# Kernel tuning notes

Measured on AMD Instinct MI355X. Metric: run time of the kernel, lower is better.

The kernel has to match this reference:

```python
import jax, jax.numpy as jnp
import numpy as np

D_MODEL = 1024
DK = 1024
DV = 1024
B, S = 8, 2048


def setup_inputs() -> dict:
    key = jax.random.key(0)
    ks = jax.random.split(key, 7)
    lim = 1.0 / np.sqrt(D_MODEL)
    x = jax.random.normal(ks[0], (B, S, D_MODEL), dtype=jnp.float32)
    Wq = jax.random.uniform(ks[1], (D_MODEL, DK), minval=-lim, maxval=lim, dtype=jnp.float32)
    bq = jax.random.uniform(ks[2], (DK,), minval=-lim, maxval=lim, dtype=jnp.float32)
    Wk = jax.random.uniform(ks[3], (D_MODEL, DK), minval=-lim, maxval=lim, dtype=jnp.float32)
    bk = jax.random.uniform(ks[4], (DK,), minval=-lim, maxval=lim, dtype=jnp.float32)
    Wv = jax.random.uniform(ks[5], (D_MODEL, DV), minval=-lim, maxval=lim, dtype=jnp.float32)
    bv = jax.random.uniform(ks[6], (DV,), minval=-lim, maxval=lim, dtype=jnp.float32)
    return {"x": x, "Wq": Wq, "bq": bq, "Wk": Wk, "bk": bk, "Wv": Wv, "bv": bv}


def reference(x, Wq, bq, Wk, bk, Wv, bv):
    # QKV projections: [B,S,d_model] -> [B,S,dk/dv]
    q = jnp.einsum('bsd,dk->bsk', x, Wq) + bq
    k = jnp.einsum('bsd,dk->bsk', x, Wk) + bk
    v = jnp.einsum('bsd,dv->bsv', x, Wv) + bv
    scale = 1.0 / jnp.sqrt(jnp.float32(DK))
    # scores: [B,S,S]
    scores = jnp.einsum('bqk,bsk->bqs', q, k) * scale
    probs = jax.nn.softmax(scores, axis=-1)
    return jnp.einsum('bqs,bsv->bqv', probs, v)
```

## Files before the change

### kernel.cpp

```cpp
#include <hip/hip_runtime.h>


#define DEV __device__ __forceinline__

typedef unsigned short u16;
typedef __attribute__((ext_vector_type(8))) short bf16x8;
typedef __attribute__((ext_vector_type(4))) float f32x4;

DEV float bf2f(u16 u) {
  unsigned v = ((unsigned)u) << 16;
  float f;
  __builtin_memcpy(&f, &v, 4);
  return f;
}
DEV u16 f2bf(float f) {
  unsigned v;
  __builtin_memcpy(&v, &f, 4);
  return (u16)((v + 0x7fffu + ((v >> 16) & 1u)) >> 16);
}

DEV void gload16(const u16* g, u16* l) {
  __builtin_amdgcn_global_load_lds(
      (const __attribute__((address_space(1))) void*)g,
      (__attribute__((address_space(3))) void*)l, 16, 0, 0);
}

#define BAR() __builtin_amdgcn_s_barrier()
#define SCHED0() __builtin_amdgcn_sched_barrier(0)
#define LGKM0() asm volatile("s_waitcnt lgkmcnt(0)" ::: "memory")
#define VMC(n) asm volatile("s_waitcnt vmcnt(" #n ")" ::: "memory")

__global__ __launch_bounds__(256) void cvt_f32_bf16(const float* __restrict__ x,
                                                    u16* __restrict__ y) {
  const long long i = ((long long)blockIdx.x * 256 + threadIdx.x) * 4;
  float4 v = *(const float4*)&x[i];
  ushort4 o;
  o.x = f2bf(v.x); o.y = f2bf(v.y); o.z = f2bf(v.z); o.w = f2bf(v.w);
  *(ushort4*)&y[i] = o;
}

__global__ __launch_bounds__(256) void transpose_cvt3(
    const float* __restrict__ Wq, const float* __restrict__ Wk,
    const float* __restrict__ Wv, u16* __restrict__ Wt) {
  __shared__ float tl[64][65];
  const float* W = blockIdx.z == 0 ? Wq : blockIdx.z == 1 ? Wk : Wv;
  u16* dst = Wt + (long long)blockIdx.z * 1048576LL;
  const int n0 = blockIdx.x * 64;
  const int k0 = blockIdx.y * 64;
  const int tid = threadIdx.x;
  const int c = tid & 31, r = tid >> 5;
#pragma unroll
  for (int i = 0; i < 8; ++i) {
    const int k = i * 8 + r;
    float2 v2 = *(const float2*)&W[(long long)(k0 + k) * 1024 + n0 + c * 2];
    tl[k][c * 2] = v2.x;
    tl[k][c * 2 + 1] = v2.y;
  }
  __syncthreads();
#pragma unroll
  for (int i = 0; i < 8; ++i) {
    const int n = i * 8 + r;
    ushort2 o;
    o.x = f2bf(tl[c * 2][n]);
    o.y = f2bf(tl[c * 2 + 1][n]);
    *(ushort2*)&dst[(long long)(n0 + n) * 1024 + k0 + c * 2] = o;
  }
}

__global__ __launch_bounds__(256) void reduce_ml(const float* __restrict__ PS,
                                                 float* __restrict__ Li) {
  const int i = blockIdx.x * 256 + threadIdx.x;
  const int z = i >> 11, r = i & 2047;
  const float* ps = PS + ((long long)(z * 8) << 11) + r;
  float L = 0.f;
#pragma unroll
  for (int p = 0; p < 8; ++p) L += ps[p << 11];
  Li[i] = 1.0f / L;
}


template <int OUT_MODE>
__global__ __launch_bounds__(512, 4) void gemm128(
    const u16* __restrict__ A, const u16* __restrict__ B,
    const float* __restrict__ bias, void* __restrict__ Cv, int K, int lda,
    int ldb, int ldc, long long bA, long long bB, long long bC, float scale,
    const float* __restrict__ pm, float* __restrict__ ps) {
  __shared__ __attribute__((aligned(16))) char smem[49152];
  const int tid = threadIdx.x;
  const int w = tid >> 6, l = tid & 63;
  const int wr = w >> 2, wc = w & 3;

  const int gx = gridDim.x, gy = gridDim.y;
  long long flat =
      blockIdx.x + (long long)gx * (blockIdx.y + (long long)gy * blockIdx.z);
  const long long nwg = (long long)gx * gy * gridDim.z;
  if ((nwg & 7) == 0) flat = (flat & 7) * (nwg >> 3) + (flat >> 3);
  const int bx = (int)(flat % gx);
  const long long rem = flat / gx;
  const int by = (int)(rem % gy);
  const int z = (int)(rem / gy);

  A += (long long)z * bA;
  B += (long long)z * bB;
  const long long tm = (long long)by * 128;
  const long long tn = (long long)bx * 256;

  const int l15 = l & 15, hi4 = l >> 4;
  const int slotc = (hi4 ^ ((l15 >> 1) & 3)) * 16;
  const char* bA0 = smem + (wr * 64 + l15) * 64 + slotc;
  const char* bB0 = smem + 8192 + (wc * 64 + l15) * 64 + slotc;

  const int srow = tid >> 2;
  const int kseg = (tid & 3) ^ ((tid >> 3) & 3);
  const int tid16 = tid * 16;
  const u16* pA = A + (tm + srow) * (long long)lda + kseg * 8;
  const u16* pB0 = B + (tn + srow) * (long long)ldb + kseg * 8;
  const u16* pB1 = B + (tn + 128 + srow) * (long long)ldb + kseg * 8;

#define STG(BO)                                           \
  gload16(pA, (u16*)(smem + (BO) + tid16));               \
  gload16(pB0, (u16*)(smem + (BO) + 8192 + tid16));       \
  gload16(pB1, (u16*)(smem + (BO) + 16384 + tid16));      \
  pA += 32;                                               \
  pB0 += 32;                                              \
  pB1 += 32;

#define RDAB(BO)                                                    \
  _Pragma("unroll") for (int mi = 0; mi < 4; ++mi)                  \
      afr[mi] = *(const bf16x8*)(bA0 + (BO) + mi * 1024);           \
  _Pragma("unroll") for (int ni = 0; ni < 4; ++ni)                  \
      bfr[ni] = *(const bf16x8*)(bB0 + (BO) + ni * 1024);

#define MFMAT()                                                          \
  __builtin_amdgcn_s_setprio(1);                                         \
  _Pragma("unroll") for (int ni = 0; ni < 4; ++ni)                       \
      _Pragma("unroll") for (int mi = 0; mi < 4; ++mi)                   \
          acc[mi][ni] = __builtin_amdgcn_mfma_f32_16x16x32_bf16(         \
              afr[mi], bfr[ni], acc[mi][ni], 0, 0, 0);                   \
  __builtin_amdgcn_s_setprio(0);

#define TILE(BO, T)                  \
  RDAB(BO);                          \
  LGKM0();                           \
  SCHED0();                          \
  BAR();                             \
  if ((T) + 2 < nt) {                \
    STG(BO);                         \
    VMC(3);                          \
  } else {                           \
    VMC(0);                          \
  }                                  \
  SCHED0();                          \
  MFMAT();                           \
  SCHED0();                          \
  BAR();

  f32x4 acc[4][4];
  const f32x4 zero = {0.f, 0.f, 0.f, 0.f};
#pragma unroll
  for (int i = 0; i < 4; ++i)
#pragma unroll
    for (int j = 0; j < 4; ++j) acc[i][j] = zero;

  bf16x8 afr[4], bfr[4];
  const int nt = K >> 5;

  STG(0);
  STG(24576);
  VMC(3);
  BAR();

  for (int t = 0; t < nt; t += 2) {
    TILE(0, t);
    TILE(24576, t + 1);
  }

  const int ro4 = (l >> 4) * 4;
  const int co = l & 15;
  if (OUT_MODE == 4) {
    float* C = (float*)Cv + (long long)z * bC;
#pragma unroll
    for (int mi = 0; mi < 4; ++mi) {
      const long long row0 = tm + wr * 64 + mi * 16 + ro4;
      float li[4];
#pragma unroll
      for (int r = 0; r < 4; ++r) li[r] = pm[(long long)z * 2048 + row0 + r];
#pragma unroll
      for (int ni = 0; ni < 4; ++ni) {
        const long long col = tn + wc * 64 + ni * 16 + co;
#pragma unroll
        for (int r = 0; r < 4; ++r)
          C[(row0 + r) * ldc + col] = acc[mi][ni][r] * li[r];
      }
    }
  } else if (OUT_MODE == 1) {
    u16* C = (u16*)Cv + (long long)z * bC;
    float* lps = (float*)smem;
#pragma unroll
    for (int mi = 0; mi < 4; ++mi) {
      const long long row0 = tm + wr * 64 + mi * 16 + ro4;
#pragma unroll
      for (int r = 0; r < 4; ++r) {
        float s_ = 0.f;
#pragma unroll
        for (int ni = 0; ni < 4; ++ni) {
          const float e = __builtin_amdgcn_exp2f(acc[mi][ni][r] * scale);
          s_ += e;
          C[(row0 + r) * ldc + tn + wc * 64 + ni * 16 + co] = f2bf(e);
        }
#pragma unroll
        for (int off = 1; off < 16; off <<= 1) s_ += __shfl_xor(s_, off, 64);
        if (co == 0) lps[(wr * 64 + mi * 16 + ro4 + r) * 4 + wc] = s_;
      }
    }
    __syncthreads();
    if (tid < 128) {
      const float S = lps[tid * 4] + lps[tid * 4 + 1] + lps[tid * 4 + 2] +
                      lps[tid * 4 + 3];
      ps[(((long long)z * 8 + bx) << 11) + tm + tid] = S;
    }
  } else {
    u16* C = (u16*)Cv + (long long)z * bC;
#pragma unroll
    for (int mi = 0; mi < 4; ++mi) {
      const long long row0 = tm + wr * 64 + mi * 16 + ro4;
#pragma unroll
      for (int ni = 0; ni < 4; ++ni) {
        const long long col = tn + wc * 64 + ni * 16 + co;
        const float badd = (OUT_MODE == 0) ? bias[col] : 0.f;
#pragma unroll
        for (int r = 0; r < 4; ++r) {
          float v = acc[mi][ni][r];
          if (OUT_MODE == 0) v += badd;
          if (OUT_MODE == 3) v += bias[row0 + r];
          C[(row0 + r) * ldc + col] = f2bf(v);
        }
      }
    }
  }
}

extern "C" void kernel_launch(void* const* d_in, const int* in_sizes, int n_in,
                              void* d_out, int out_size, void* d_ws,
                              size_t ws_size, hipStream_t stream) {
  const float* x = (const float*)d_in[0];
  const float* Wq = (const float*)d_in[1];
  const float* bq = (const float*)d_in[2];
  const float* Wk = (const float*)d_in[3];
  const float* bk = (const float*)d_in[4];
  const float* Wv = (const float*)d_in[5];
  const float* bv = (const float*)d_in[6];
  float* out = (float*)d_out;

  const long long MT = 16384LL;
  const long long D = 1024LL;

  u16* ws = (u16*)d_ws;
  u16* Wt = ws;
  u16* Q = Wt + 3 * 1048576LL;
  u16* Kb = Q + MT * D;
  u16* Vt = Kb + MT * D;
  u16* SC = Vt + MT * D;
  u16* xb = SC;
  float* PSa = (float*)d_ws;
  float* Li = PSa + 131072;

  const float cl2e = 1.4426950408889634f * 0.03125f;

  cvt_f32_bf16<<<dim3(16384), dim3(256), 0, stream>>>(x, xb);
  transpose_cvt3<<<dim3(16, 16, 3), dim3(256), 0, stream>>>(Wq, Wk, Wv, Wt);
  gemm128<0><<<dim3(4, 128, 1), dim3(512), 0, stream>>>(
      xb, Wt, bq, Q, 1024, 1024, 1024, 1024, 0, 0, 0, 0.f, nullptr, nullptr);
  gemm128<0><<<dim3(4, 128, 1), dim3(512), 0, stream>>>(
      xb, Wt + 1048576LL, bk, Kb, 1024, 1024, 1024, 1024, 0, 0, 0, 0.f,
      nullptr, nullptr);
  gemm128<3><<<dim3(64, 8, 1), dim3(512), 0, stream>>>(
      Wt + 2097152LL, xb, bv, Vt, 1024, 1024, 1024, 16384, 0, 0, 0, 0.f,
      nullptr, nullptr);
  gemm128<1><<<dim3(8, 16, 8), dim3(512), 0, stream>>>(
      Q, Kb, nullptr, SC, 1024, 1024, 1024, 2048, 2048 * 1024LL, 2048 * 1024LL,
      2048LL * 2048LL, cl2e, nullptr, PSa);
  reduce_ml<<<dim3(64), dim3(256), 0, stream>>>(PSa, Li);
  gemm128<4><<<dim3(4, 16, 8), dim3(512), 0, stream>>>(
      SC, Vt, nullptr, out, 2048, 2048, 16384, 1024, 2048LL * 2048LL, 2048LL,
      2048 * 1024LL, 0.f, Li, nullptr);
}
```

Baseline: 299.5 us.

## Switch GEMMs to 32x32x16 MFMA, merge prep kernels and Q/K launches

The GEMM inner loop moves from 16x16x32 bf16 MFMAs to 32x32x16 MFMAs, with 2x2 f32x16 accumulators per wave. LDS fragment reads and all epilogues are remapped to the 32x32 output layout, which needs fewer LDS reads per flop and fewer MFMA issues. The x conversion and the weight transpose-convert are fused into one prep kernel. The Q and K projections run as one batched launch, with the bias pointer picked by z. The 32-lane row layout changes how stores coalesce in the epilogues, and the softmax row sum now needs a wider shuffle reduction.

```diff
diff --git a/kernel.cpp b/kernel.cpp
--- a/kernel.cpp
+++ b/kernel.cpp
@@ -5,7 +5,7 @@
 
 typedef unsigned short u16;
 typedef __attribute__((ext_vector_type(8))) short bf16x8;
-typedef __attribute__((ext_vector_type(4))) float f32x4;
+typedef __attribute__((ext_vector_type(16))) float f32x16;
 
 DEV float bf2f(u16 u) {
   unsigned v = ((unsigned)u) << 16;
@@ -30,24 +30,27 @@
 #define LGKM0() asm volatile("s_waitcnt lgkmcnt(0)" ::: "memory")
 #define VMC(n) asm volatile("s_waitcnt vmcnt(" #n ")" ::: "memory")
 
-__global__ __launch_bounds__(256) void cvt_f32_bf16(const float* __restrict__ x,
-                                                    u16* __restrict__ y) {
-  const long long i = ((long long)blockIdx.x * 256 + threadIdx.x) * 4;
-  float4 v = *(const float4*)&x[i];
-  ushort4 o;
-  o.x = f2bf(v.x); o.y = f2bf(v.y); o.z = f2bf(v.z); o.w = f2bf(v.w);
-  *(ushort4*)&y[i] = o;
-}
-
-__global__ __launch_bounds__(256) void transpose_cvt3(
-    const float* __restrict__ Wq, const float* __restrict__ Wk,
-    const float* __restrict__ Wv, u16* __restrict__ Wt) {
+__global__ __launch_bounds__(256) void prep(const float* __restrict__ x,
+                                            const float* __restrict__ Wq,
+                                            const float* __restrict__ Wk,
+                                            const float* __restrict__ Wv,
+                                            u16* __restrict__ xb,
+                                            u16* __restrict__ Wt) {
   __shared__ float tl[64][65];
-  const float* W = blockIdx.z == 0 ? Wq : blockIdx.z == 1 ? Wk : Wv;
-  u16* dst = Wt + (long long)blockIdx.z * 1048576LL;
-  const int n0 = blockIdx.x * 64;
-  const int k0 = blockIdx.y * 64;
   const int tid = threadIdx.x;
+  if (blockIdx.x < 16384) {
+    const long long i = ((long long)blockIdx.x * 256 + tid) * 4;
+    float4 v = *(const float4*)&x[i];
+    ushort4 o;
+    o.x = f2bf(v.x); o.y = f2bf(v.y); o.z = f2bf(v.z); o.w = f2bf(v.w);
+    *(ushort4*)&xb[i] = o;
+    return;
+  }
+  const int b = blockIdx.x - 16384;
+  const int bz = b >> 8, byk = (b >> 4) & 15, bxn = b & 15;
+  const float* W = bz == 0 ? Wq : bz == 1 ? Wk : Wv;
+  u16* dst = Wt + (long long)bz * 1048576LL;
+  const int n0 = bxn * 64, k0 = byk * 64;
   const int c = tid & 31, r = tid >> 5;
 #pragma unroll
   for (int i = 0; i < 8; ++i) {
@@ -80,7 +83,7 @@
 
 
 template <int OUT_MODE>
-__global__ __launch_bounds__(512, 4) void gemm128(
+__global__ __launch_bounds__(512, 4) void gemm32(
     const u16* __restrict__ A, const u16* __restrict__ B,
     const float* __restrict__ bias, void* __restrict__ Cv, int K, int lda,
     int ldb, int ldc, long long bA, long long bB, long long bC, float scale,
@@ -105,10 +108,12 @@
   const long long tm = (long long)by * 128;
   const long long tn = (long long)bx * 256;
 
-  const int l15 = l & 15, hi4 = l >> 4;
-  const int slotc = (hi4 ^ ((l15 >> 1) & 3)) * 16;
-  const char* bA0 = smem + (wr * 64 + l15) * 64 + slotc;
-  const char* bB0 = smem + 8192 + (wc * 64 + l15) * 64 + slotc;
+  const int l31 = l & 31, h = l >> 5;
+  const int xsw = (l31 >> 1) & 3;
+  const int sl0 = ((0 * 2 + h) ^ xsw) * 16;
+  const int sl1 = ((1 * 2 + h) ^ xsw) * 16;
+  const char* bAr = smem + (wr * 64 + l31) * 64;
+  const char* bBr = smem + 8192 + (wc * 64 + l31) * 64;
 
   const int srow = tid >> 2;
   const int kseg = (tid & 3) ^ ((tid >> 3) & 3);
@@ -125,18 +130,25 @@
   pB0 += 32;                                              \
   pB1 += 32;
 
-#define RDAB(BO)                                                    \
-  _Pragma("unroll") for (int mi = 0; mi < 4; ++mi)                  \
-      afr[mi] = *(const bf16x8*)(bA0 + (BO) + mi * 1024);           \
-  _Pragma("unroll") for (int ni = 0; ni < 4; ++ni)                  \
-      bfr[ni] = *(const bf16x8*)(bB0 + (BO) + ni * 1024);
-
-#define MFMAT()                                                          \
-  __builtin_amdgcn_s_setprio(1);                                         \
-  _Pragma("unroll") for (int ni = 0; ni < 4; ++ni)                       \
-      _Pragma("unroll") for (int mi = 0; mi < 4; ++mi)                   \
-          acc[mi][ni] = __builtin_amdgcn_mfma_f32_16x16x32_bf16(         \
-              afr[mi], bfr[ni], acc[mi][ni], 0, 0, 0);                   \
+#define RDAB(BO)                                            \
+  afr[0][0] = *(const bf16x8*)(bAr + (BO) + sl0);           \
+  afr[0][1] = *(const bf16x8*)(bAr + (BO) + sl1);           \
+  afr[1][0] = *(const bf16x8*)(bAr + (BO) + 2048 + sl0);    \
+  afr[1][1] = *(const bf16x8*)(bAr + (BO) + 2048 + sl1);    \
+  bfr[0][0] = *(const bf16x8*)(bBr + (BO) + sl0);           \
+  bfr[0][1] = *(const bf16x8*)(bBr + (BO) + sl1);           \
+  bfr[1][0] = *(const bf16x8*)(bBr + (BO) + 2048 + sl0);    \
+  bfr[1][1] = *(const bf16x8*)(bBr + (BO) + 2048 + sl1);
+
+#define MFMAT()                                                           \
+  __builtin_amdgcn_s_setprio(1);                                          \
+  _Pragma("unroll") for (int ni = 0; ni < 2; ++ni)                        \
+      _Pragma("unroll") for (int mi = 0; mi < 2; ++mi) {                  \
+    acc[mi][ni] = __builtin_amdgcn_mfma_f32_32x32x16_bf16(                \
+        afr[mi][0], bfr[ni][0], acc[mi][ni], 0, 0, 0);                    \
+    acc[mi][ni] = __builtin_amdgcn_mfma_f32_32x32x16_bf16(                \
+        afr[mi][1], bfr[ni][1], acc[mi][ni], 0, 0, 0);                    \
+  }                                                                       \
   __builtin_amdgcn_s_setprio(0);
 
 #define TILE(BO, T)                  \
@@ -155,14 +167,15 @@
   SCHED0();                          \
   BAR();
 
-  f32x4 acc[4][4];
-  const f32x4 zero = {0.f, 0.f, 0.f, 0.f};
-#pragma unroll
-  for (int i = 0; i < 4; ++i)
-#pragma unroll
-    for (int j = 0; j < 4; ++j) acc[i][j] = zero;
-
-  bf16x8 afr[4], bfr[4];
+  f32x16 acc[2][2];
+#pragma unroll
+  for (int i = 0; i < 2; ++i)
+#pragma unroll
+    for (int j = 0; j < 2; ++j)
+#pragma unroll
+      for (int e = 0; e < 16; ++e) acc[i][j][e] = 0.f;
+
+  bf16x8 afr[2][2], bfr[2][2];
   const int nt = K >> 5;
 
   STG(0);
@@ -175,42 +188,45 @@
     TILE(24576, t + 1);
   }
 
-  const int ro4 = (l >> 4) * 4;
-  const int co = l & 15;
   if (OUT_MODE == 4) {
     float* C = (float*)Cv + (long long)z * bC;
 #pragma unroll
-    for (int mi = 0; mi < 4; ++mi) {
-      const long long row0 = tm + wr * 64 + mi * 16 + ro4;
-      float li[4];
-#pragma unroll
-      for (int r = 0; r < 4; ++r) li[r] = pm[(long long)z * 2048 + row0 + r];
-#pragma unroll
-      for (int ni = 0; ni < 4; ++ni) {
-        const long long col = tn + wc * 64 + ni * 16 + co;
-#pragma unroll
-        for (int r = 0; r < 4; ++r)
-          C[(row0 + r) * ldc + col] = acc[mi][ni][r] * li[r];
+    for (int mi = 0; mi < 2; ++mi) {
+      const long long rb = tm + wr * 64 + mi * 32;
+      float lir[16];
+#pragma unroll
+      for (int rg = 0; rg < 16; ++rg)
+        lir[rg] = pm[(long long)z * 2048 + rb + (rg & 3) + 8 * (rg >> 2) + 4 * h];
+#pragma unroll
+      for (int ni = 0; ni < 2; ++ni) {
+        const long long col = tn + wc * 64 + ni * 32 + l31;
+#pragma unroll
+        for (int rg = 0; rg < 16; ++rg) {
+          const long long row = rb + (rg & 3) + 8 * (rg >> 2) + 4 * h;
+          C[row * ldc + col] = acc[mi][ni][rg] * lir[rg];
+        }
       }
     }
   } else if (OUT_MODE == 1) {
     u16* C = (u16*)Cv + (long long)z * bC;
     float* lps = (float*)smem;
 #pragma unroll
-    for (int mi = 0; mi < 4; ++mi) {
-      const long long row0 = tm + wr * 64 + mi * 16 + ro4;
-#pragma unroll
-      for (int r = 0; r < 4; ++r) {
+    for (int mi = 0; mi < 2; ++mi) {
+      const long long rb = tm + wr * 64 + mi * 32;
+#pragma unroll
+      for (int rg = 0; rg < 16; ++rg) {
+        const int rloc = (rg & 3) + 8 * (rg >> 2) + 4 * h;
+        const long long row = rb + rloc;
         float s_ = 0.f;
 #pragma unroll
-        for (int ni = 0; ni < 4; ++ni) {
-          const float e = __builtin_amdgcn_exp2f(acc[mi][ni][r] * scale);
+        for (int ni = 0; ni < 2; ++ni) {
+          const float e = __builtin_amdgcn_exp2f(acc[mi][ni][rg] * scale);
           s_ += e;
-          C[(row0 + r) * ldc + tn + wc * 64 + ni * 16 + co] = f2bf(e);
+          C[row * ldc + tn + wc * 64 + ni * 32 + l31] = f2bf(e);
         }
 #pragma unroll
-        for (int off = 1; off < 16; off <<= 1) s_ += __shfl_xor(s_, off, 64);
-        if (co == 0) lps[(wr * 64 + mi * 16 + ro4 + r) * 4 + wc] = s_;
+        for (int off = 1; off < 32; off <<= 1) s_ += __shfl_xor(s_, off, 64);
+        if (l31 == 0) lps[(wr * 64 + mi * 32 + rloc) * 4 + wc] = s_;
       }
     }
     __syncthreads();
@@ -219,21 +235,36 @@
                       lps[tid * 4 + 3];
       ps[(((long long)z * 8 + bx) << 11) + tm + tid] = S;
     }
+  } else if (OUT_MODE == 0) {
+    u16* C = (u16*)Cv + (long long)z * bC;
+    const float* bb = z ? pm : bias;
+#pragma unroll
+    for (int mi = 0; mi < 2; ++mi) {
+      const long long rb = tm + wr * 64 + mi * 32;
+#pragma unroll
+      for (int ni = 0; ni < 2; ++ni) {
+        const long long col = tn + wc * 64 + ni * 32 + l31;
+        const float badd = bb[col];
+#pragma unroll
+        for (int rg = 0; rg < 16; ++rg) {
+          const long long row = rb + (rg & 3) + 8 * (rg >> 2) + 4 * h;
+          C[row * ldc + col] = f2bf(acc[mi][ni][rg] + badd);
+        }
+      }
+    }
   } else {
     u16* C = (u16*)Cv + (long long)z * bC;
 #pragma unroll
-    for (int mi = 0; mi < 4; ++mi) {
-      const long long row0 = tm + wr * 64 + mi * 16 + ro4;
-#pragma unroll
-      for (int ni = 0; ni < 4; ++ni) {
-        const long long col = tn + wc * 64 + ni * 16 + co;
-        const float badd = (OUT_MODE == 0) ? bias[col] : 0.f;
-#pragma unroll
-        for (int r = 0; r < 4; ++r) {
-          float v = acc[mi][ni][r];
-          if (OUT_MODE == 0) v += badd;
-          if (OUT_MODE == 3) v += bias[row0 + r];
-          C[(row0 + r) * ldc + col] = f2bf(v);
+    for (int mi = 0; mi < 2; ++mi) {
+      const long long rb = tm + wr * 64 + mi * 32;
+#pragma unroll
+      for (int rg = 0; rg < 16; ++rg) {
+        const long long row = rb + (rg & 3) + 8 * (rg >> 2) + 4 * h;
+        const float badd = bias[row];
+#pragma unroll
+        for (int ni = 0; ni < 2; ++ni) {
+          const long long col = tn + wc * 64 + ni * 32 + l31;
+          C[row * ldc + col] = f2bf(acc[mi][ni][rg] + badd);
         }
       }
     }
@@ -267,21 +298,18 @@
 
   const float cl2e = 1.4426950408889634f * 0.03125f;
 
-  cvt_f32_bf16<<<dim3(16384), dim3(256), 0, stream>>>(x, xb);
-  transpose_cvt3<<<dim3(16, 16, 3), dim3(256), 0, stream>>>(Wq, Wk, Wv, Wt);
-  gemm128<0><<<dim3(4, 128, 1), dim3(512), 0, stream>>>(
-      xb, Wt, bq, Q, 1024, 1024, 1024, 1024, 0, 0, 0, 0.f, nullptr, nullptr);
-  gemm128<0><<<dim3(4, 128, 1), dim3(512), 0, stream>>>(
-      xb, Wt + 1048576LL, bk, Kb, 1024, 1024, 1024, 1024, 0, 0, 0, 0.f,
-      nullptr, nullptr);
-  gemm128<3><<<dim3(64, 8, 1), dim3(512), 0, stream>>>(
+  prep<<<dim3(16384 + 768), dim3(256), 0, stream>>>(x, Wq, Wk, Wv, xb, Wt);
+  gemm32<0><<<dim3(4, 128, 2), dim3(512), 0, stream>>>(
+      xb, Wt, bq, Q, 1024, 1024, 1024, 1024, 0, 1048576LL, 16777216LL, 0.f,
+      bk, nullptr);
+  gemm32<3><<<dim3(64, 8, 1), dim3(512), 0, stream>>>(
       Wt + 2097152LL, xb, bv, Vt, 1024, 1024, 1024, 16384, 0, 0, 0, 0.f,
       nullptr, nullptr);
-  gemm128<1><<<dim3(8, 16, 8), dim3(512), 0, stream>>>(
+  gemm32<1><<<dim3(8, 16, 8), dim3(512), 0, stream>>>(
       Q, Kb, nullptr, SC, 1024, 1024, 1024, 2048, 2048 * 1024LL, 2048 * 1024LL,
       2048LL * 2048LL, cl2e, nullptr, PSa);
   reduce_ml<<<dim3(64), dim3(256), 0, stream>>>(PSa, Li);
-  gemm128<4><<<dim3(4, 16, 8), dim3(512), 0, stream>>>(
+  gemm32<4><<<dim3(4, 16, 8), dim3(512), 0, stream>>>(
       SC, Vt, nullptr, out, 2048, 2048, 16384, 1024, 2048LL * 2048LL, 2048LL,
       2048 * 1024LL, 0.f, Li, nullptr);
 }
```

Measured after the change: 318.6 us. +6.4%, slower.
